# Kernel tuning notes

Measured on AMD Instinct MI355X. Metric: run time of the kernel, lower is better.

The kernel has to match this reference:

```python
import jax, jax.numpy as jnp
import numpy as np

MD = 40                 # max_displacement
K = 2 * MD + 1          # 81 kernel size -> K*K = 6561 displacements


def setup_inputs() -> dict:
    key = jax.random.key(0)
    k1, k2 = jax.random.split(key)
    b, c, h, w = 2, 128, 64, 96
    x1 = jax.random.normal(k1, (b, c, h, w), dtype=jnp.float32)
    x2 = jax.random.normal(k2, (b, c, h, w), dtype=jnp.float32)
    return {"x1": x1, "x2": x2}


def reference(x1, x2):
    b, c, h, w = x1.shape
    # zero-pad x2 by MD on each spatial side (matches F.pad(x2, (pad,)*4))
    x2p = jnp.pad(x2, ((0, 0), (0, 0), (MD, MD), (MD, MD)))

    # Fused sliding-window correlation: scan over the K*K displacements,
    # slicing a (b,c,h,w) window of x2p and reducing over channels.
    # Avoids the (b,c,K^2,h,w) unfold blow-up entirely.
    def step(carry, s):
        dy = s // K
        dx = s % K
        win = jax.lax.dynamic_slice(x2p, (0, 0, dy, dx), (b, c, h, w))
        return carry, jnp.einsum('bchw,bchw->bhw', x1, win)

    _, corr = jax.lax.scan(step, None, jnp.arange(K * K))  # (K*K, b, h, w)
    corr = jnp.transpose(corr, (1, 0, 2, 3))               # (b, K*K, h, w)
    return corr / jnp.sqrt(jnp.float32(c))
```

## Files before the change

### kernel.cpp

```cpp
#include <hip/hip_runtime.h>

#define CH    128
#define HH    64
#define WW    96
#define MD    40
#define KD    81
#define HW    (HH*WW)
#define CHW   (CH*HW)
#define SCALE 0.08838834764831845f
#define LSTR  72
#define CHUNK (WW*LSTR)
#define WS2_USH ((size_t)2*HH*2*CHUNK)

typedef __attribute__((ext_vector_type(8))) short bf16x8;
typedef __attribute__((ext_vector_type(4))) float f32x4;

__device__ inline unsigned int pack2bf(float lo, float hi) {
    unsigned int a = __float_as_uint(lo), b = __float_as_uint(hi);
    a = (a + 0x7FFFu + ((a >> 16) & 1u)) >> 16;
    b = (b + 0x7FFFu + ((b >> 16) & 1u)) >> 16;
    return a | (b << 16);
}

__device__ __forceinline__ void gload16(const void* g, void* l) {
    __builtin_amdgcn_global_load_lds(
        (const __attribute__((address_space(1))) void*)g,
        (__attribute__((address_space(3))) void*)l, 16, 0, 0);
}

__global__ __launch_bounds__(256) void prepack(
    const float* __restrict__ x1, const float* __restrict__ x2,
    unsigned short* __restrict__ ws)
{
    const int y = blockIdx.x;
    const int h = blockIdx.y & 1;
    const int t = blockIdx.y >> 1;
    const int b = blockIdx.z;

    const float* src = (t ? x2 : x1)
        + (size_t)b * CHW + (size_t)(h * 64) * HW + (size_t)y * WW;
    unsigned short* dst = ws + (size_t)t * WS2_USH
        + ((size_t)(b * HH + y) * 2 + h) * CHUNK;

    for (int j = threadIdx.x; j < 8 * WW; j += 256) {
        const int cg = j / WW;
        const int x  = j - cg * WW;
        const float* p = src + (size_t)(cg * 8) * HW + x;
        float f[8];
        #pragma unroll
        for (int i = 0; i < 8; ++i) f[i] = p[(size_t)i * HW];
        uint4 w;
        w.x = pack2bf(f[0], f[1]); w.y = pack2bf(f[2], f[3]);
        w.z = pack2bf(f[4], f[5]); w.w = pack2bf(f[6], f[7]);
        *reinterpret_cast<uint4*>(&dst[(size_t)x * LSTR + cg * 8]) = w;
    }
}

__global__ __launch_bounds__(256, 4) void corr_kernel(
    const unsigned short* __restrict__ ws, float* __restrict__ out)
{
    const int y   = blockIdx.x;
    const int dy  = blockIdx.y;
    const int b   = blockIdx.z;
    const int tid = threadIdx.x;

    float* outbase = out + ((size_t)b * (KD * KD) + (size_t)dy * KD) * HW
                         + (size_t)y * WW;

    const int y2 = y + dy - MD;
    if (y2 < 0 || y2 >= HH) {
        const float4 z = make_float4(0.f, 0.f, 0.f, 0.f);
        for (int f = tid; f < KD * (WW / 4); f += 256) {
            const int dx = f / (WW / 4);
            const int x4 = f - dx * (WW / 4);
            *reinterpret_cast<float4*>(outbase + (size_t)dx * HW + x4 * 4) = z;
        }
        return;
    }

    __shared__ __align__(16) char smem[WW * WW * 4];
    unsigned short* sStage = reinterpret_cast<unsigned short*>(smem);
    unsigned short* sA = sStage;
    unsigned short* sB = sStage + CHUNK;
    float*          sG = reinterpret_cast<float*>(smem);

    const unsigned short* wsA = ws + ((size_t)(b * HH + y ) * 2) * CHUNK;
    const unsigned short* wsB = ws + WS2_USH + ((size_t)(b * HH + y2) * 2) * CHUNK;

    const int lane = tid & 63;
    const int wave = tid >> 6;
    const int m0   = (wave >> 1) * 48;
    const int n0   = (wave & 1) * 48;
    const int lr   = lane & 15;
    const int q    = lane >> 4;

    f32x4 acc[3][3];
    #pragma unroll
    for (int i = 0; i < 3; ++i)
        #pragma unroll
        for (int j = 0; j < 3; ++j)
            acc[i][j] = (f32x4){0.f, 0.f, 0.f, 0.f};

    for (int h = 0; h < 2; ++h) {
        if (h) __syncthreads();
        const unsigned short* g1 = wsA + (size_t)h * CHUNK;
        const unsigned short* g2 = wsB + (size_t)h * CHUNK;
        #pragma unroll
        for (int it = 0; it < 7; ++it) {
            const int idx = it * 256 + tid;
            if (idx < 2 * (CHUNK / 8)) {
                const unsigned short* g = (idx < (CHUNK / 8))
                    ? g1 + (size_t)idx * 8
                    : g2 + (size_t)(idx - (CHUNK / 8)) * 8;
                gload16(g, sStage + (size_t)idx * 8);
            }
        }
        __syncthreads();

        #pragma unroll
        for (int kk = 0; kk < 2; ++kk) {
            const int cl = kk * 32 + q * 8;
            bf16x8 af[3], bg[3];
            #pragma unroll
            for (int i = 0; i < 3; ++i)
                af[i] = *reinterpret_cast<const bf16x8*>(&sB[(m0 + 16 * i + lr) * LSTR + cl]);
            #pragma unroll
            for (int j = 0; j < 3; ++j)
                bg[j] = *reinterpret_cast<const bf16x8*>(&sA[(n0 + 16 * j + lr) * LSTR + cl]);
            #pragma unroll
            for (int i = 0; i < 3; ++i)
                #pragma unroll
                for (int j = 0; j < 3; ++j)
                    acc[i][j] = __builtin_amdgcn_mfma_f32_16x16x32_bf16(
                        af[i], bg[j], acc[i][j], 0, 0, 0);
        }
    }

    __syncthreads();
    #pragma unroll
    for (int i = 0; i < 3; ++i) {
        #pragma unroll
        for (int j = 0; j < 3; ++j) {
            const int col  = n0 + 16 * j + lr;
            const int rowb = m0 + 16 * i + q * 4;
            #pragma unroll
            for (int r = 0; r < 4; ++r) {
                const int row = rowb + r;
                sG[(row * WW + col) ^ ((row & 7) << 2)] = acc[i][j][r];
            }
        }
    }
    __syncthreads();

    int dx = tid / WW;
    int x  = tid - dx * WW;
    #pragma unroll 1
    for (int it = 0; it < 31; ++it) {
        if (dx < KD) {
            const int x2v   = x + dx - MD;
            const bool valid = ((unsigned)x2v < (unsigned)WW);
            const int w     = valid ? ((x2v * WW + x) ^ ((x2v & 7) << 2)) : 0;
            float v = sG[w] * SCALE;
            v = valid ? v : 0.f;
            outbase[(size_t)(dx * HW + x)] = v;
        }
        x += 64; dx += 2;
        if (x >= WW) { x -= WW; ++dx; }
    }
}

extern "C" void kernel_launch(void* const* d_in, const int* in_sizes, int n_in,
                              void* d_out, int out_size, void* d_ws, size_t ws_size,
                              hipStream_t stream) {
    const float* x1 = (const float*)d_in[0];
    const float* x2 = (const float*)d_in[1];
    float* out = (float*)d_out;
    unsigned short* ws = (unsigned short*)d_ws;

    hipLaunchKernelGGL(prepack, dim3(HH, 4, 2), dim3(256), 0, stream, x1, x2, ws);

    dim3 g(HH, KD, 2);
    hipLaunchKernelGGL(corr_kernel, g, dim3(256), 0, stream, ws, out);
}
```

Baseline: 353.0 us.

## Prefetch second channel half into registers and remap blocks across XCDs

```diff
diff --git a/kernel.cpp b/kernel.cpp
--- a/kernel.cpp
+++ b/kernel.cpp
@@ -11,6 +11,8 @@
 #define LSTR  72
 #define CHUNK (WW*LSTR)
 #define WS2_USH ((size_t)2*HH*2*CHUNK)
+#define NWG   (HH*KD*2)
+#define CPX   (NWG/8)
 
 typedef __attribute__((ext_vector_type(8))) short bf16x8;
 typedef __attribute__((ext_vector_type(4))) float f32x4;
@@ -56,12 +58,38 @@
     }
 }
 
+__device__ __forceinline__ void mfma_half(
+    const unsigned short* sA, const unsigned short* sB,
+    int m0, int n0, int lr, int q, f32x4 (&acc)[3][3])
+{
+    #pragma unroll
+    for (int kk = 0; kk < 2; ++kk) {
+        const int cl = kk * 32 + q * 8;
+        bf16x8 af[3], bg[3];
+        #pragma unroll
+        for (int i = 0; i < 3; ++i)
+            af[i] = *reinterpret_cast<const bf16x8*>(&sB[(m0 + 16 * i + lr) * LSTR + cl]);
+        #pragma unroll
+        for (int j = 0; j < 3; ++j)
+            bg[j] = *reinterpret_cast<const bf16x8*>(&sA[(n0 + 16 * j + lr) * LSTR + cl]);
+        #pragma unroll
+        for (int i = 0; i < 3; ++i)
+            #pragma unroll
+            for (int j = 0; j < 3; ++j)
+                acc[i][j] = __builtin_amdgcn_mfma_f32_16x16x32_bf16(
+                    af[i], bg[j], acc[i][j], 0, 0, 0);
+    }
+}
+
 __global__ __launch_bounds__(256, 4) void corr_kernel(
     const unsigned short* __restrict__ ws, float* __restrict__ out)
 {
-    const int y   = blockIdx.x;
-    const int dy  = blockIdx.y;
-    const int b   = blockIdx.z;
+    const int bid = blockIdx.x;
+    const int wg  = (bid & 7) * CPX + (bid >> 3);
+    const int b   = (wg >= HH * KD) ? 1 : 0;
+    const int rem = wg - b * (HH * KD);
+    const int dy  = rem >> 6;
+    const int y   = rem & 63;
     const int tid = threadIdx.x;
 
     float* outbase = out + ((size_t)b * (KD * KD) + (size_t)dy * KD) * HW
@@ -94,47 +122,51 @@
     const int lr   = lane & 15;
     const int q    = lane >> 4;
 
-    f32x4 acc[3][3];
-    #pragma unroll
-    for (int i = 0; i < 3; ++i)
-        #pragma unroll
-        for (int j = 0; j < 3; ++j)
-            acc[i][j] = (f32x4){0.f, 0.f, 0.f, 0.f};
-
-    for (int h = 0; h < 2; ++h) {
-        if (h) __syncthreads();
-        const unsigned short* g1 = wsA + (size_t)h * CHUNK;
-        const unsigned short* g2 = wsB + (size_t)h * CHUNK;
+    #pragma unroll
+    for (int it = 0; it < 7; ++it) {
+        const int idx = it * 256 + tid;
+        if (idx < 2 * (CHUNK / 8)) {
+            const unsigned short* g = (idx < (CHUNK / 8))
+                ? wsA + (size_t)idx * 8
+                : wsB + (size_t)(idx - (CHUNK / 8)) * 8;
+            gload16(g, sStage + (size_t)idx * 8);
+        }
+    }
+    uint4 pf[7];
+    {
+        const unsigned short* g1b = wsA + CHUNK;
+        const unsigned short* g2b = wsB + CHUNK;
         #pragma unroll
         for (int it = 0; it < 7; ++it) {
             const int idx = it * 256 + tid;
             if (idx < 2 * (CHUNK / 8)) {
                 const unsigned short* g = (idx < (CHUNK / 8))
-                    ? g1 + (size_t)idx * 8
-                    : g2 + (size_t)(idx - (CHUNK / 8)) * 8;
-                gload16(g, sStage + (size_t)idx * 8);
+                    ? g1b + (size_t)idx * 8
+                    : g2b + (size_t)(idx - (CHUNK / 8)) * 8;
+                pf[it] = *reinterpret_cast<const uint4*>(g);
             }
         }
-        __syncthreads();
-
-        #pragma unroll
-        for (int kk = 0; kk < 2; ++kk) {
-            const int cl = kk * 32 + q * 8;
-            bf16x8 af[3], bg[3];
-            #pragma unroll
-            for (int i = 0; i < 3; ++i)
-                af[i] = *reinterpret_cast<const bf16x8*>(&sB[(m0 + 16 * i + lr) * LSTR + cl]);
-            #pragma unroll
-            for (int j = 0; j < 3; ++j)
-                bg[j] = *reinterpret_cast<const bf16x8*>(&sA[(n0 + 16 * j + lr) * LSTR + cl]);
-            #pragma unroll
-            for (int i = 0; i < 3; ++i)
-                #pragma unroll
-                for (int j = 0; j < 3; ++j)
-                    acc[i][j] = __builtin_amdgcn_mfma_f32_16x16x32_bf16(
-                        af[i], bg[j], acc[i][j], 0, 0, 0);
-        }
-    }
+    }
+
+    f32x4 acc[3][3];
+    #pragma unroll
+    for (int i = 0; i < 3; ++i)
+        #pragma unroll
+        for (int j = 0; j < 3; ++j)
+            acc[i][j] = (f32x4){0.f, 0.f, 0.f, 0.f};
+
+    __syncthreads();
+    mfma_half(sA, sB, m0, n0, lr, q, acc);
+    __syncthreads();
+
+    #pragma unroll
+    for (int it = 0; it < 7; ++it) {
+        const int idx = it * 256 + tid;
+        if (idx < 2 * (CHUNK / 8))
+            *reinterpret_cast<uint4*>(sStage + (size_t)idx * 8) = pf[it];
+    }
+    __syncthreads();
+    mfma_half(sA, sB, m0, n0, lr, q, acc);
 
     __syncthreads();
     #pragma unroll
@@ -179,6 +211,5 @@
 
     hipLaunchKernelGGL(prepack, dim3(HH, 4, 2), dim3(256), 0, stream, x1, x2, ws);
 
-    dim3 g(HH, KD, 2);
-    hipLaunchKernelGGL(corr_kernel, g, dim3(256), 0, stream, ws, out);
-}
+    hipLaunchKernelGGL(corr_kernel, dim3(NWG), dim3(256), 0, stream, ws, out);
+}
```

After: 424.9 us. 1.2x slower.

## Store correlation in dx-major LDS layout and write float4 outputs with XCD-aware block mapping

Applied to the files above, without the earlier changes.

```diff
diff --git a/kernel.cpp b/kernel.cpp
--- a/kernel.cpp
+++ b/kernel.cpp
@@ -11,6 +11,8 @@
 #define LSTR  72
 #define CHUNK (WW*LSTR)
 #define WS2_USH ((size_t)2*HH*2*CHUNK)
+#define NWG   (HH*KD*2)
+#define CPX   (NWG/8)
 
 typedef __attribute__((ext_vector_type(8))) short bf16x8;
 typedef __attribute__((ext_vector_type(4))) float f32x4;
@@ -56,12 +58,38 @@
     }
 }
 
+__device__ __forceinline__ void mfma_half(
+    const unsigned short* sA, const unsigned short* sB,
+    int m0, int n0, int lr, int q, f32x4 (&acc)[3][3])
+{
+    #pragma unroll
+    for (int kk = 0; kk < 2; ++kk) {
+        const int cl = kk * 32 + q * 8;
+        bf16x8 af[3], bg[3];
+        #pragma unroll
+        for (int i = 0; i < 3; ++i)
+            af[i] = *reinterpret_cast<const bf16x8*>(&sB[(m0 + 16 * i + lr) * LSTR + cl]);
+        #pragma unroll
+        for (int j = 0; j < 3; ++j)
+            bg[j] = *reinterpret_cast<const bf16x8*>(&sA[(n0 + 16 * j + lr) * LSTR + cl]);
+        #pragma unroll
+        for (int i = 0; i < 3; ++i)
+            #pragma unroll
+            for (int j = 0; j < 3; ++j)
+                acc[i][j] = __builtin_amdgcn_mfma_f32_16x16x32_bf16(
+                    af[i], bg[j], acc[i][j], 0, 0, 0);
+    }
+}
+
 __global__ __launch_bounds__(256, 4) void corr_kernel(
     const unsigned short* __restrict__ ws, float* __restrict__ out)
 {
-    const int y   = blockIdx.x;
-    const int dy  = blockIdx.y;
-    const int b   = blockIdx.z;
+    const int bid = blockIdx.x;
+    const int wg  = (bid & 7) * CPX + (bid >> 3);
+    const int b   = (wg >= HH * KD) ? 1 : 0;
+    const int rem = wg - b * (HH * KD);
+    const int dy  = rem >> 6;
+    const int y   = rem & 63;
     const int tid = threadIdx.x;
 
     float* outbase = out + ((size_t)b * (KD * KD) + (size_t)dy * KD) * HW
@@ -70,15 +98,19 @@
     const int y2 = y + dy - MD;
     if (y2 < 0 || y2 >= HH) {
         const float4 z = make_float4(0.f, 0.f, 0.f, 0.f);
-        for (int f = tid; f < KD * (WW / 4); f += 256) {
-            const int dx = f / (WW / 4);
-            const int x4 = f - dx * (WW / 4);
-            *reinterpret_cast<float4*>(outbase + (size_t)dx * HW + x4 * 4) = z;
+        #pragma unroll
+        for (int it = 0; it < 8; ++it) {
+            const int idx = it * 256 + tid;
+            if (idx < KD * (WW / 4)) {
+                const int dx = idx / 24;
+                const int x4 = idx - dx * 24;
+                *reinterpret_cast<float4*>(outbase + (size_t)dx * HW + x4 * 4) = z;
+            }
         }
         return;
     }
 
-    __shared__ __align__(16) char smem[WW * WW * 4];
+    __shared__ __align__(16) char smem[KD * WW * 4];
     unsigned short* sStage = reinterpret_cast<unsigned short*>(smem);
     unsigned short* sA = sStage;
     unsigned short* sB = sStage + CHUNK;
@@ -117,23 +149,7 @@
         }
         __syncthreads();
 
-        #pragma unroll
-        for (int kk = 0; kk < 2; ++kk) {
-            const int cl = kk * 32 + q * 8;
-            bf16x8 af[3], bg[3];
-            #pragma unroll
-            for (int i = 0; i < 3; ++i)
-                af[i] = *reinterpret_cast<const bf16x8*>(&sB[(m0 + 16 * i + lr) * LSTR + cl]);
-            #pragma unroll
-            for (int j = 0; j < 3; ++j)
-                bg[j] = *reinterpret_cast<const bf16x8*>(&sA[(n0 + 16 * j + lr) * LSTR + cl]);
-            #pragma unroll
-            for (int i = 0; i < 3; ++i)
-                #pragma unroll
-                for (int j = 0; j < 3; ++j)
-                    acc[i][j] = __builtin_amdgcn_mfma_f32_16x16x32_bf16(
-                        af[i], bg[j], acc[i][j], 0, 0, 0);
-        }
+        mfma_half(sA, sB, m0, n0, lr, q, acc);
     }
 
     __syncthreads();
@@ -145,26 +161,31 @@
             const int rowb = m0 + 16 * i + q * 4;
             #pragma unroll
             for (int r = 0; r < 4; ++r) {
-                const int row = rowb + r;
-                sG[(row * WW + col) ^ ((row & 7) << 2)] = acc[i][j][r];
+                const int dxv = (rowb + r) - col + MD;
+                if ((unsigned)dxv < (unsigned)KD) {
+                    const int w = (dxv * WW + col) ^ (((dxv >> 2) & 1) << 4);
+                    sG[w] = acc[i][j][r] * SCALE;
+                }
             }
         }
     }
     __syncthreads();
 
-    int dx = tid / WW;
-    int x  = tid - dx * WW;
-    #pragma unroll 1
-    for (int it = 0; it < 31; ++it) {
-        if (dx < KD) {
-            const int x2v   = x + dx - MD;
-            const bool valid = ((unsigned)x2v < (unsigned)WW);
-            const int w     = valid ? ((x2v * WW + x) ^ ((x2v & 7) << 2)) : 0;
-            float v = sG[w] * SCALE;
-            v = valid ? v : 0.f;
-            outbase[(size_t)(dx * HW + x)] = v;
-        }
-        x += 64; dx += 2;
+    int dx = tid / 24;
+    int x  = 4 * tid - dx * WW;
+    #pragma unroll
+    for (int it = 0; it < 8; ++it) {
+        if (it < 7 || tid < 152) {
+            const int baddr = ((dx * WW + x) << 2) ^ (((dx >> 2) & 1) << 6);
+            float4 v = *reinterpret_cast<const float4*>(smem + baddr);
+            const int x2b = x + dx - MD;
+            v.x = ((unsigned)(x2b + 0) < (unsigned)WW) ? v.x : 0.f;
+            v.y = ((unsigned)(x2b + 1) < (unsigned)WW) ? v.y : 0.f;
+            v.z = ((unsigned)(x2b + 2) < (unsigned)WW) ? v.z : 0.f;
+            v.w = ((unsigned)(x2b + 3) < (unsigned)WW) ? v.w : 0.f;
+            *reinterpret_cast<float4*>(outbase + (size_t)(dx * HW + x)) = v;
+        }
+        x += 64; dx += 10;
         if (x >= WW) { x -= WW; ++dx; }
     }
 }
@@ -179,6 +200,5 @@
 
     hipLaunchKernelGGL(prepack, dim3(HH, 4, 2), dim3(256), 0, stream, x1, x2, ws);
 
-    dim3 g(HH, KD, 2);
-    hipLaunchKernelGGL(corr_kernel, g, dim3(256), 0, stream, ws, out);
-}
+    hipLaunchKernelGGL(corr_kernel, dim3(NWG), dim3(256), 0, stream, ws, out);
+}
```

After: 346.8 us. About the same (-1.8%).
